# Kernel optimization log

Measured on AMD Instinct MI355X. Metric: run time of the kernel, lower is better.

## Reference

```python
import jax, jax.numpy as jnp
import numpy as np

Q = 8192      # num query tokens
S = 32768     # num support points
E = 131072    # num edges (query<-support neighbor pairs)
D = 256       # token_dim
H = 8         # num_heads
HD = D // H   # head_dim = 32
GEO = 128     # geo mlp_hidden = geo_dim
FFN = 2 * D   # ffn hidden
STAT_IN = 12  # 4 stats * 3 coords
EPS_LN = 1e-5


def gelu(x):
    return jax.nn.gelu(x, approximate=False)  # torch nn.GELU default (erf)


def layernorm(x, g, b):
    m = jnp.mean(x, axis=-1, keepdims=True)
    v = jnp.mean((x - m) ** 2, axis=-1, keepdims=True)
    return (x - m) * jax.lax.rsqrt(v + EPS_LN) * g + b


def setup_inputs() -> dict:
    key = jax.random.key(0)
    ks = jax.random.split(key, 16)
    w = lambda k, shp: jax.random.normal(k, shp, jnp.float32) * 0.02
    return {
        "query_tokens": jax.random.normal(ks[0], (Q, D), jnp.float32),
        "query_pos": jax.random.normal(ks[1], (Q, 3), jnp.float32),
        "support_feats": jax.random.normal(ks[2], (S, D), jnp.float32),
        "support_pos": jax.random.normal(ks[3], (S, 3), jnp.float32),
        "Wq": w(ks[4], (D, D)), "Wk": w(ks[5], (D, D)), "Wv": w(ks[6], (D, D)),
        "Wg": w(ks[7], (GEO, D)),
        "Wo": w(ks[8], (D, D)), "bo": jnp.zeros((D,), jnp.float32),
        "log_tau": jnp.array(0.0, jnp.float32),
        "ln1_g": jnp.ones((D,), jnp.float32), "ln1_b": jnp.zeros((D,), jnp.float32),
        "ln2_g": jnp.ones((D,), jnp.float32), "ln2_b": jnp.zeros((D,), jnp.float32),
        "Wf1": w(ks[9], (D, FFN)), "bf1": jnp.zeros((FFN,), jnp.float32),
        "Wf2": w(ks[10], (FFN, D)), "bf2": jnp.zeros((D,), jnp.float32),
        "Gw1": w(ks[11], (STAT_IN, GEO)), "Gb1": jnp.zeros((GEO,), jnp.float32),
        "Gw2": w(ks[12], (GEO, GEO)), "Gb2": jnp.zeros((GEO,), jnp.float32),
        "q_idx": jnp.sort(jax.random.randint(ks[13], (E,), 0, Q)),
        "s_idx": jax.random.randint(ks[14], (E,), 0, S),
        "num_queries": Q,
    }


def geo_stats(rel, q_idx, num_q):
    # rel: [E,3] relative positions; segmented mean/std/min/max -> [num_q, 12]
    ones = jnp.ones((rel.shape[0], 1), rel.dtype)
    cnt = jnp.maximum(jax.ops.segment_sum(ones, q_idx, num_q), 1.0)  # [Q,1]
    mean = jax.ops.segment_sum(rel, q_idx, num_q) / cnt
    var = jax.ops.segment_sum((rel - mean[q_idx]) ** 2, q_idx, num_q) / cnt
    std = jnp.sqrt(var)
    # torch inits min/max with +/-inf then clamps to [-100,100]; jax segment
    # min/max init with dtype extremes -> same result after clip
    mn = jnp.clip(jax.ops.segment_min(rel, q_idx, num_q), -100.0, 100.0)
    mx = jnp.clip(jax.ops.segment_max(rel, q_idx, num_q), -100.0, 100.0)
    return jnp.concatenate([mean, std, mn, mx], axis=-1)


def reference(query_tokens, query_pos, support_feats, support_pos,
              Wq, Wk, Wv, Wg, Wo, bo, log_tau,
              ln1_g, ln1_b, ln2_g, ln2_b,
              Wf1, bf1, Wf2, bf2, Gw1, Gb1, Gw2, Gb2,
              q_idx, s_idx, num_queries):
    num_q = num_queries
    # ---- statistical geo embedding ----
    rel = support_pos[s_idx] - query_pos[q_idx]                 # [E,3]
    raw = geo_stats(rel, q_idx, num_q)                          # [Q,12]
    geo = gelu(gelu(raw @ Gw1 + Gb1) @ Gw2 + Gb2)               # [Q,GEO]

    # ---- AGNO cross attention (pre-norm) ----
    qt = layernorm(query_tokens, ln1_g, ln1_b)
    Qf = qt @ Wq                                                # [Q,D]
    Kf = support_feats @ Wk                                     # [S,D]
    Vf = support_feats @ Wv                                     # [S,D]
    Gf = geo @ Wg                                               # [Q,D]
    qh = Qf[q_idx].reshape(E, H, HD)
    kh = Kf[s_idx].reshape(E, H, HD)
    vh = Vf[s_idx].reshape(E, H, HD)
    gh = Gf[q_idx].reshape(E, H, HD)
    tau = jnp.exp(log_tau)
    scores = jnp.sum(qh * kh, axis=-1) / (jnp.sqrt(jnp.float32(HD)) * tau)  # [E,H]
    # torch scores_max starts at 0 -> max(0, segment max)
    smax = jnp.maximum(jax.ops.segment_max(scores, q_idx, num_q), 0.0)
    ex = jnp.exp(scores - smax[q_idx])
    ssum = jax.ops.segment_sum(ex, q_idx, num_q)
    alpha = ex / jnp.maximum(ssum[q_idx], 1e-8)                 # [E,H]
    weighted = alpha[..., None] * (vh + gh)                     # [E,H,HD]
    out = jax.ops.segment_sum(weighted, q_idx, num_q)           # [Q,H,HD]
    attn = out.reshape(num_q, D) @ Wo + bo

    # ---- residual + FFN ----
    x = query_tokens + attn
    x = x + gelu(layernorm(x, ln2_g, ln2_b) @ Wf1 + bf1) @ Wf2 + bf2
    return x
```

## Files before the change

kernel.cpp:

```cpp
#include <hip/hip_runtime.h>
#include <math.h>

#define QN 8192
#define SN 32768
#define EN 131072
#define DN 256
#define HN 8
#define HDN 32
#define GEON 128
#define FFNN 512

typedef __attribute__((ext_vector_type(8))) short bf16x8;
typedef __attribute__((ext_vector_type(8))) unsigned short u16x8;
typedef __attribute__((ext_vector_type(4))) float f32x4;

__device__ __forceinline__ unsigned short f2b(float f) {
  union { float f; unsigned u; } v; v.f = f;
  unsigned u = v.u;
  u += 0x7fffu + ((u >> 16) & 1u);
  return (unsigned short)(u >> 16);
}
__device__ __forceinline__ float b2f(unsigned short h) {
  union { unsigned u; float f; } v; v.u = ((unsigned)h) << 16; return v.f;
}
// ... 34 lines not shown
    int k0 = (tile % ktiles) * 64, n0 = (tile / ktiles) * 64;
    int c4 = (t & 15) * 4;
    int r = t >> 4;
#pragma unroll
    for (int p = 0; p < 4; ++p) {
      int row = p * 16 + r;
      float4 v = *(const float4*)(src + (size_t)(k0 + row) * N + n0 + c4);
      ts[row][c4 + 0] = v.x; ts[row][c4 + 1] = v.y;
      ts[row][c4 + 2] = v.z; ts[row][c4 + 3] = v.w;
    }
    __syncthreads();
#pragma unroll
    for (int p = 0; p < 4; ++p) {
      int n = p * 16 + r;
      ushort4 o;
      o.x = f2b(ts[c4 + 0][n]); o.y = f2b(ts[c4 + 1][n]);
      o.z = f2b(ts[c4 + 2][n]); o.w = f2b(ts[c4 + 3][n]);
      *(ushort4*)(dst + (size_t)(n0 + n) * K + k0 + c4) = o;
    }
  } else if (b < 169) {
    int i = (b - 136) * 256 + t;
    if (i > QN) return;
    int lo = 0, hi = EN;
    while (lo < hi) {
      int mid = (lo + hi) >> 1;
      if (q_idx[mid] < i) lo = mid + 1; else hi = mid;
    }
    offs[i] = lo;
  } else {
    int row = (b - 169) * 4 + (t >> 6);
    int lane = t & 63;
    const float* xr = x_ln + (size_t)row * DN;
    float4 v = *(const float4*)(xr + lane * 4);
    float s = v.x + v.y + v.z + v.w;
    float ss = v.x * v.x + v.y * v.y + v.z * v.z + v.w * v.w;
#pragma unroll
    for (int msk = 1; msk <= 32; msk <<= 1) {
      s += __shfl_xor(s, msk);
      ss += __shfl_xor(ss, msk);
    }
    float mean = s * (1.f / 256.f);
    float var = ss * (1.f / 256.f) - mean * mean;
    float rs = 1.0f / sqrtf(var + 1e-5f);
    float4 gg = *(const float4*)(lng + lane * 4);
    float4 bb = *(const float4*)(lnb + lane * 4);
    unsigned short* o = ln_out + (size_t)row * DN + lane * 4;
    o[0] = f2b((v.x - mean) * rs * gg.x + bb.x);
    o[1] = f2b((v.y - mean) * rs * gg.y + bb.y);
    o[2] = f2b((v.z - mean) * rs * gg.z + bb.z);
    o[3] = f2b((v.w - mean) * rs * gg.w + bb.w);
  }
}

__global__ __launch_bounds__(256) void ln_kernel(
    const float* x, const float* g, const float* b, unsigned short* out) {
  int row = blockIdx.x * 4 + (threadIdx.x >> 6);
  int lane = threadIdx.x & 63;
  const float* xr = x + (size_t)row * DN;
  float4 v = *(const float4*)(xr + lane * 4);
  float s = v.x + v.y + v.z + v.w;
  float ss = v.x * v.x + v.y * v.y + v.z * v.z + v.w * v.w;
#pragma unroll
  for (int msk = 1; msk <= 32; msk <<= 1) {
    s += __shfl_xor(s, msk);
    ss += __shfl_xor(ss, msk);
  }
  float mean = s * (1.f / 256.f);
  float var = ss * (1.f / 256.f) - mean * mean;
  float rs = 1.0f / sqrtf(var + 1e-5f);
  float4 gg = *(const float4*)(g + lane * 4);
  float4 bb = *(const float4*)(b + lane * 4);
  unsigned short* o = out + (size_t)row * DN + lane * 4;
  o[0] = f2b((v.x - mean) * rs * gg.x + bb.x);
  o[1] = f2b((v.y - mean) * rs * gg.y + bb.y);
  o[2] = f2b((v.z - mean) * rs * gg.z + bb.z);
  o[3] = f2b((v.w - mean) * rs * gg.w + bb.w);
}


__device__ __forceinline__ void kv_body(
    char* smem, const float* A, const unsigned short* BT, unsigned short* KVb,
    int bm, int t) {
  unsigned short* As = (unsigned short*)smem;
  unsigned short* Bs = (unsigned short*)(smem + 32768);
  int w = t >> 6, lane = t & 63;
  int quad = lane >> 4, l16 = lane & 15;
  int wr = w >> 1, wc = w & 1;
  int srow = t >> 2, sub = t & 3;
  {
    const float* Ag = A + (size_t)(bm + srow) * 256 + sub * 64;
#pragma unroll
    for (int i = 0; i < 8; ++i) {
      float4 f0 = *(const float4*)(Ag + i * 8);
      float4 f1 = *(const float4*)(Ag + i * 8 + 4);
      u16x8 u;
      u[0] = f2b(f0.x); u[1] = f2b(f0.y); u[2] = f2b(f0.z); u[3] = f2b(f0.w);
      u[4] = f2b(f1.x); u[5] = f2b(f1.y); u[6] = f2b(f1.z); u[7] = f2b(f1.w);
      *lds_gk<256>(As, srow, sub * 64 + i * 8) = u;
    }
  }
  int brow = t >> 3, bsub = t & 7;
  u16x8 pre[4];
  {
    const unsigned short* Bg = BT + (size_t)brow * 256 + bsub * 32;
#pragma unroll
    for (int i = 0; i < 4; ++i) pre[i] = *reinterpret_cast<const u16x8*>(Bg + i * 8);
  }
  for (int ct = 0; ct < 16; ++ct) {
#pragma unroll
    for (int i = 0; i < 4; ++i)
      *lds_gk<256>(Bs, brow, bsub * 32 + i * 8) = pre[i];
    __syncthreads();
    if (ct < 15) {
      const unsigned short* Bg = BT + (size_t)((ct + 1) * 32 + brow) * 256 + bsub * 32;
#pragma unroll
      for (int i = 0; i < 4; ++i) pre[i] = *reinterpret_cast<const u16x8*>(Bg + i * 8);
    }
    f32x4 acc[2];
    acc[0] = (f32x4){0.f, 0.f, 0.f, 0.f};
    acc[1] = (f32x4){0.f, 0.f, 0.f, 0.f};
#pragma unroll
    for (int k = 0; k < 8; ++k) {
      bf16x8 a0 = *reinterpret_cast<bf16x8*>(lds_gk<256>(As, wr * 32 + l16, k * 32 + quad * 8));
      bf16x8 a1 = *reinterpret_cast<bf16x8*>(lds_gk<256>(As, wr * 32 + 16 + l16, k * 32 + quad * 8));
      bf16x8 b0 = *reinterpret_cast<bf16x8*>(lds_gk<256>(Bs, wc * 16 + l16, k * 32 + quad * 8));
      acc[0] = __builtin_amdgcn_mfma_f32_16x16x32_bf16(a0, b0, acc[0], 0, 0, 0);
      acc[1] = __builtin_amdgcn_mfma_f32_16x16x32_bf16(a1, b0, acc[1], 0, 0, 0);
    }
#pragma unroll
    for (int i = 0; i < 2; ++i)
#pragma unroll
      for (int r = 0; r < 4; ++r) {
        int rw = bm + wr * 32 + i * 16 + quad * 4 + r;
        int col = ct * 32 + wc * 16 + l16;
        KVb[(size_t)rw * 512 + col] = f2b(acc[i][r]);
      }
    __syncthreads();
  }
}

template <bool A_FP32, bool HAS_BIAS, bool DO_GELU, bool HAS_RESID, bool STORE_F32>
__device__ __forceinline__ void gemm64_body(
    char* smem, const void* Ap, const unsigned short* BT, int N, int K,
    const float* bias, const float* resid, float* outF, unsigned short* outB,
    int bm, int bn, int t) {
  unsigned short (*As)[40] = (unsigned short(*)[40])smem;
  unsigned short (*Bs)[40] = (unsigned short(*)[40])(smem + 5120);
  int w = t >> 6, lane = t & 63;
  int wr = w >> 1, wc = w & 1;
  int quad = lane >> 4, l16 = lane & 15;
  int row = t >> 2, chunk = t & 3;

  const float* AgF = (const float*)Ap + (size_t)(bm + row) * K + chunk * 8;
  const unsigned short* AgB = (const unsigned short*)Ap + (size_t)(bm + row) * K + chunk * 8;
  const unsigned short* Bg = BT + (size_t)(bn + row) * K + chunk * 8;

  float4 pf0, pf1;
  u16x8 pa, pb;
  if (A_FP32) { pf0 = *(const float4*)AgF; pf1 = *(const float4*)(AgF + 4); }
  else        { pa = *(const u16x8*)AgB; }
  pb = *(const u16x8*)Bg;

  f32x4 acc[2][2];
#pragma unroll
  for (int i = 0; i < 2; ++i)
#pragma unroll
    for (int j = 0; j < 2; ++j) acc[i][j] = (f32x4){0.f, 0.f, 0.f, 0.f};

  for (int k0 = 0; k0 < K; k0 += 32) {
    u16x8 ua;
    if (A_FP32) {
      ua[0] = f2b(pf0.x); ua[1] = f2b(pf0.y); ua[2] = f2b(pf0.z); ua[3] = f2b(pf0.w);
      ua[4] = f2b(pf1.x); ua[5] = f2b(pf1.y); ua[6] = f2b(pf1.z); ua[7] = f2b(pf1.w);
    } else {
      ua = pa;
    }
    *reinterpret_cast<u16x8*>(&As[row][chunk * 8]) = ua;
    *reinterpret_cast<u16x8*>(&Bs[row][chunk * 8]) = pb;
    __syncthreads();
    if (k0 + 32 < K) {
      if (A_FP32) { pf0 = *(const float4*)(AgF + k0 + 32); pf1 = *(const float4*)(AgF + k0 + 36); }
      else        { pa = *(const u16x8*)(AgB + k0 + 32); }
      pb = *(const u16x8*)(Bg + k0 + 32);
    }
    bf16x8 a0 = *reinterpret_cast<const bf16x8*>(&As[wr * 32 + l16][quad * 8]);
    bf16x8 a1 = *reinterpret_cast<const bf16x8*>(&As[wr * 32 + 16 + l16][quad * 8]);
    bf16x8 b0 = *reinterpret_cast<const bf16x8*>(&Bs[wc * 32 + l16][quad * 8]);
    bf16x8 b1 = *reinterpret_cast<const bf16x8*>(&Bs[wc * 32 + 16 + l16][quad * 8]);
    acc[0][0] = __builtin_amdgcn_mfma_f32_16x16x32_bf16(a0, b0, acc[0][0], 0, 0, 0);
    acc[0][1] = __builtin_amdgcn_mfma_f32_16x16x32_bf16(a0, b1, acc[0][1], 0, 0, 0);
    acc[1][0] = __builtin_amdgcn_mfma_f32_16x16x32_bf16(a1, b0, acc[1][0], 0, 0, 0);
    acc[1][1] = __builtin_amdgcn_mfma_f32_16x16x32_bf16(a1, b1, acc[1][1], 0, 0, 0);
    __syncthreads();
  }

#pragma unroll
  for (int i = 0; i < 2; ++i)
#pragma unroll
    for (int j = 0; j < 2; ++j) {
      int col = bn + wc * 32 + j * 16 + l16;
      float bv = HAS_BIAS ? bias[col] : 0.f;
#pragma unroll
      for (int r = 0; r < 4; ++r) {
        int rw = bm + wr * 32 + i * 16 + quad * 4 + r;
        float v = acc[i][j][r] + bv;
        if (DO_GELU) v = gelu_f(v);
        if (HAS_RESID) v += resid[(size_t)rw * N + col];
        if (STORE_F32) outF[(size_t)rw * N + col] = v;
        else outB[(size_t)rw * N + col] = f2b(v);
      }
    }
}

__device__ __forceinline__ void geo_body(
    char* smem, const float* qpos, const float* spos, const int* offs,
    const int* s_idx, const float* Gw1, const float* Gb1,
    const float* Gw2, const float* Gb2, const unsigned short* WgT,
    unsigned short* Gf_b, int qb, int t) {
  float (*rs)[12] = (float(*)[12])smem;
  unsigned short* geoL = (unsigned short*)(smem + 3072);
  float (*h1)[128] = (float(*)[128])(smem + 19456);
  unsigned short* Bs = (unsigned short*)(smem + 19456);

  {
    int q = qb + (t >> 2);
    int sub = t & 3;
    int e0 = offs[q], e1 = offs[q + 1];
    float qx = qpos[q * 3 + 0], qy = qpos[q * 3 + 1], qz = qpos[q * 3 + 2];
    float cnt = 0.f, sx = 0.f, sy = 0.f, sz = 0.f, sxx = 0.f, syy = 0.f, szz = 0.f;
    float mnx = 1e30f, mny = 1e30f, mnz = 1e30f, mxx = -1e30f, mxy = -1e30f, mxz = -1e30f;
    for (int e = e0 + sub; e < e1; e += 4) {
      int s = s_idx[e];
      float rx = spos[s * 3 + 0] - qx;
      float ry = spos[s * 3 + 1] - qy;
      float rz = spos[s * 3 + 2] - qz;
      cnt += 1.f;
      sx += rx; sy += ry; sz += rz;
      sxx += rx * rx; syy += ry * ry; szz += rz * rz;
      mnx = fminf(mnx, rx); mny = fminf(mny, ry); mnz = fminf(mnz, rz);
      mxx = fmaxf(mxx, rx); mxy = fmaxf(mxy, ry); mxz = fmaxf(mxz, rz);
    }
#pragma unroll
    for (int msk = 1; msk <= 2; msk <<= 1) {
      cnt += __shfl_xor(cnt, msk);
      sx += __shfl_xor(sx, msk); sy += __shfl_xor(sy, msk); sz += __shfl_xor(sz, msk);
      sxx += __shfl_xor(sxx, msk); syy += __shfl_xor(syy, msk); szz += __shfl_xor(szz, msk);
      mnx = fminf(mnx, __shfl_xor(mnx, msk));
      mny = fminf(mny, __shfl_xor(mny, msk));
      mnz = fminf(mnz, __shfl_xor(mnz, msk));
      mxx = fmaxf(mxx, __shfl_xor(mxx, msk));
      mxy = fmaxf(mxy, __shfl_xor(mxy, msk));
      mxz = fmaxf(mxz, __shfl_xor(mxz, msk));
    }
    if (sub == 0) {
      int qq = t >> 2;
      float c = fmaxf(cnt, 1.f);
      float mx_ = sx / c, my_ = sy / c, mz_ = sz / c;
      float vx = fmaxf(sxx / c - mx_ * mx_, 0.f);
      float vy = fmaxf(syy / c - my_ * my_, 0.f);
      float vz = fmaxf(szz / c - mz_ * mz_, 0.f);
      rs[qq][0] = mx_; rs[qq][1] = my_; rs[qq][2] = mz_;
      rs[qq][3] = sqrtf(vx); rs[qq][4] = sqrtf(vy); rs[qq][5] = sqrtf(vz);
      rs[qq][6] = fminf(fmaxf(mnx, -100.f), 100.f);
      rs[qq][7] = fminf(fmaxf(mny, -100.f), 100.f);
      rs[qq][8] = fminf(fmaxf(mnz, -100.f), 100.f);
      rs[qq][9] = fminf(fmaxf(mxx, -100.f), 100.f);
      rs[qq][10] = fminf(fmaxf(mxy, -100.f), 100.f);
      rs[qq][11] = fminf(fmaxf(mxz, -100.f), 100.f);
    }
  }
  __syncthreads();

  {
    int j = t & 127;
    int grp = t >> 7;
    int qbase = grp * 32;
    float acc[32];
    float b1 = Gb1[j];
#pragma unroll
    for (int qq = 0; qq < 32; ++qq) acc[qq] = b1;
    for (int i = 0; i < 12; ++i) {
      float wv = Gw1[i * GEON + j];
#pragma unroll
      for (int qq = 0; qq < 32; ++qq) acc[qq] += rs[qbase + qq][i] * wv;
    }
#pragma unroll
    for (int qq = 0; qq < 32; ++qq) h1[qbase + qq][j] = gelu_f(acc[qq]);
    __syncthreads();
    float b2 = Gb2[j];
    float acc2[32];
#pragma unroll
    for (int qq = 0; qq < 32; ++qq) acc2[qq] = b2;
    for (int k = 0; k < 128; ++k) {
      float wv = Gw2[k * GEON + j];
#pragma unroll
      for (int qq = 0; qq < 32; ++qq) acc2[qq] += h1[qbase + qq][k] * wv;
    }
#pragma unroll
    for (int qq = 0; qq < 32; ++qq)
      *lds_gs128(geoL, qbase + qq, j) = f2b(gelu_f(acc2[qq]));
  }
  __syncthreads();

  {
    int w = t >> 6, lane = t & 63;
    int wr = w >> 1, wc = w & 1;
    int quad = lane >> 4, l16 = lane & 15;
    int row = t >> 2, sub = t & 3;
    for (int ct = 0; ct < 4; ++ct) {
      int bn = ct * 64;
      {
        const unsigned short* Bg = WgT + (size_t)(bn + row) * 128 + sub * 32;
#pragma unroll
        for (int i = 0; i < 4; ++i)
          *lds_gk<128>(Bs, row, sub * 32 + i * 8) = *reinterpret_cast<const u16x8*>(Bg + i * 8);
      }
      __syncthreads();
      f32x4 acc[2][2];
#pragma unroll
      for (int i = 0; i < 2; ++i)
#pragma unroll
        for (int j = 0; j < 2; ++j) acc[i][j] = (f32x4){0.f, 0.f, 0.f, 0.f};
#pragma unroll
      for (int k = 0; k < 4; ++k) {
        bf16x8 a0 = *reinterpret_cast<bf16x8*>(lds_gk<128>(geoL, wr * 32 + l16, k * 32 + quad * 8));
        bf16x8 a1 = *reinterpret_cast<bf16x8*>(lds_gk<128>(geoL, wr * 32 + 16 + l16, k * 32 + quad * 8));
        bf16x8 b0 = *reinterpret_cast<bf16x8*>(lds_gk<128>(Bs, wc * 32 + l16, k * 32 + quad * 8));
        bf16x8 b1 = *reinterpret_cast<bf16x8*>(lds_gk<128>(Bs, wc * 32 + 16 + l16, k * 32 + quad * 8));
        acc[0][0] = __builtin_amdgcn_mfma_f32_16x16x32_bf16(a0, b0, acc[0][0], 0, 0, 0);
        acc[0][1] = __builtin_amdgcn_mfma_f32_16x16x32_bf16(a0, b1, acc[0][1], 0, 0, 0);
        acc[1][0] = __builtin_amdgcn_mfma_f32_16x16x32_bf16(a1, b0, acc[1][0], 0, 0, 0);
        acc[1][1] = __builtin_amdgcn_mfma_f32_16x16x32_bf16(a1, b1, acc[1][1], 0, 0, 0);
      }
#pragma unroll
      for (int i = 0; i < 2; ++i)
#pragma unroll
        for (int j = 0; j < 2; ++j) {
          int col = bn + wc * 32 + j * 16 + l16;
#pragma unroll
          for (int r = 0; r < 4; ++r) {
            int rw = qb + wr * 32 + i * 16 + quad * 4 + r;
            Gf_b[(size_t)rw * 256 + col] = f2b(acc[i][j][r]);
          }
        }
      __syncthreads();
    }
  }
}

__global__ __launch_bounds__(256) void fused_stage2(
    const float* qpos, const float* spos, const int* offs, const int* s_idx,
    const float* Gw1, const float* Gb1, const float* Gw2, const float* Gb2,
    const unsigned short* WgT, unsigned short* Gf_b,
    const float* support_feats, const unsigned short* WkvT, unsigned short* KVb,
    const unsigned short* qt_b, const unsigned short* WqT, unsigned short* Qb) {
  __shared__ __align__(16) char smem[52224];
  int b = blockIdx.x;
  int t = threadIdx.x;
  if (b < 128) {
    geo_body(smem, qpos, spos, offs, s_idx, Gw1, Gb1, Gw2, Gb2, WgT, Gf_b, b * 64, t);
  } else if (b < 640) {
    kv_body(smem, support_feats, WkvT, KVb, (b - 128) * 64, t);
  } else {
    int bb = b - 640;
    int bm = (bb & 127) * 64, bn = (bb >> 7) * 64;
    gemm64_body<false, false, false, false, false>(
        smem, qt_b, WqT, DN, 256, nullptr, nullptr, nullptr, Qb, bm, bn, t);
  }
}

template <bool A_FP32, bool HAS_BIAS, bool DO_GELU, bool HAS_RESID, bool STORE_F32>
__global__ __launch_bounds__(256) void gemm64(
    const void* Ap, const unsigned short* BT, int N, int K,
    const float* bias, const float* resid, float* outF, unsigned short* outB) {
  __shared__ __align__(16) char smem[10240];
  gemm64_body<A_FP32, HAS_BIAS, DO_GELU, HAS_RESID, STORE_F32>(
      smem, Ap, BT, N, K, bias, resid, outF, outB,
      blockIdx.x * 64, blockIdx.y * 64, threadIdx.x);
}

__global__ __launch_bounds__(256) void attn_edge_kernel(
    const unsigned short* Qb, const unsigned short* Gfb, const unsigned short* KVb,
    const int* s_idx, const int* offs, const float* log_tau, unsigned short* attn_b) {
  int q = blockIdx.x * 4 + (threadIdx.x >> 6);
  int lane = threadIdx.x & 63;
  int slot = lane >> 4;
  int sl = lane & 15;
  int d0 = sl * 16;
  int e0 = offs[q], e1 = offs[q + 1];
  float invs = expf(-log_tau[0]) * 0.17677669529663687f;
  u16x8 qu0 = *(const u16x8*)(Qb + (size_t)q * DN + d0);
  u16x8 qu1 = *(const u16x8*)(Qb + (size_t)q * DN + d0 + 8);
  u16x8 gu0 = *(const u16x8*)(Gfb + (size_t)q * DN + d0);
  u16x8 gu1 = *(const u16x8*)(Gfb + (size_t)q * DN + d0 + 8);
  float qf[16], gf[16];
#pragma unroll
  for (int j = 0; j < 8; ++j) {
    qf[j] = b2f(qu0[j]) * invs; qf[j + 8] = b2f(qu1[j]) * invs;
    gf[j] = b2f(gu0[j]);        gf[j + 8] = b2f(gu1[j]);
  }
  const float NEG = -1e30f;
  float m = -INFINITY, l = 0.f;
  float a[16];
#pragma unroll
  for (int j = 0; j < 16; ++j) a[j] = 0.f;
  for (int e = e0; e < e1; e += 4) {
    int ee = e + slot;
    bool valid = ee < e1;
    int s = s_idx[valid ? ee : (e1 - 1)];
    const unsigned short* kr = KVb + (size_t)s * 512 + d0;
    u16x8 ku0 = *(const u16x8*)kr;
    u16x8 ku1 = *(const u16x8*)(kr + 8);
    u16x8 vu0 = *(const u16x8*)(kr + 256);
    u16x8 vu1 = *(const u16x8*)(kr + 264);
    float p = 0.f;
#pragma unroll
    for (int j = 0; j < 8; ++j) {
      p += qf[j] * b2f(ku0[j]);
      p += qf[j + 8] * b2f(ku1[j]);
    }
    p += __shfl_xor(p, 1);
    if (!valid) p = -INFINITY;
    float mnew = fmaxf(m, p);
    float sc = (m > NEG) ? __expf(m - mnew) : 0.f;
    float we = valid ? __expf(p - mnew) : 0.f;
    l = l * sc + we;
#pragma unroll
    for (int j = 0; j < 8; ++j) {
      a[j] = a[j] * sc + we * b2f(vu0[j]);
      a[j + 8] = a[j + 8] * sc + we * b2f(vu1[j]);
    }
    m = mnew;
  }
#pragma unroll
  for (int msk = 16; msk <= 32; msk <<= 1) {
    float om = __shfl_xor(m, msk);
    float ol = __shfl_xor(l, msk);
    float M2 = fmaxf(m, om);
    float ws = (m > NEG) ? __expf(m - M2) : 0.f;
    float wo = (om > NEG) ? __expf(om - M2) : 0.f;
    l = l * ws + ol * wo;
#pragma unroll
    for (int j = 0; j < 16; ++j) {
      float oa = __shfl_xor(a[j], msk);
      a[j] = a[j] * ws + oa * wo;
    }
    m = M2;
  }
  float M = fmaxf(m, 0.f);
  float em = (m > NEG) ? __expf(m - M) : 0.f;
  float denom = fmaxf(l * em, 1e-8f);
  float f = em / denom;
  float sa = l * f;
  if (slot == 0) {
    u16x8 o0, o1;
#pragma unroll
    for (int j = 0; j < 8; ++j) {
      o0[j] = f2b(a[j] * f + gf[j] * sa);
      o1[j] = f2b(a[j + 8] * f + gf[j + 8] * sa);
    }
    *(u16x8*)(attn_b + (size_t)q * DN + d0) = o0;
    *(u16x8*)(attn_b + (size_t)q * DN + d0 + 8) = o1;
  }
}

extern "C" void kernel_launch(void* const* d_in, const int* in_sizes, int n_in,
                              void* d_out, int out_size, void* d_ws, size_t ws_size,
                              hipStream_t stream) {
  const float* query_tokens  = (const float*)d_in[0];
  const float* query_pos     = (const float*)d_in[1];
  const float* support_feats = (const float*)d_in[2];
  const float* support_pos   = (const float*)d_in[3];
  const float* Wq  = (const float*)d_in[4];
  const float* Wk  = (const float*)d_in[5];
  const float* Wv  = (const float*)d_in[6];
  const float* Wg  = (const float*)d_in[7];
  const float* Wo  = (const float*)d_in[8];
  const float* bo  = (const float*)d_in[9];
  const float* log_tau = (const float*)d_in[10];
  const float* ln1_g = (const float*)d_in[11];
  const float* ln1_b = (const float*)d_in[12];
  const float* ln2_g = (const float*)d_in[13];
  const float* ln2_b = (const float*)d_in[14];
  const float* Wf1 = (const float*)d_in[15];
  const float* bf1 = (const float*)d_in[16];
  const float* Wf2 = (const float*)d_in[17];
  const float* bf2 = (const float*)d_in[18];
  const float* Gw1 = (const float*)d_in[19];
  const float* Gb1 = (const float*)d_in[20];
  const float* Gw2 = (const float*)d_in[21];
  const float* Gb2 = (const float*)d_in[22];
  const int* q_idx = (const int*)d_in[23];
  const int* s_idx = (const int*)d_in[24];
  float* out = (float*)d_out;

  char* ws = (char*)d_ws;
  size_t off = 0;
  auto alloc = [&](size_t bytes) -> void* {
    void* p = ws + off;
    off = (off + bytes + 255) & ~(size_t)255;
    return p;
  };
  unsigned short* WqT  = (unsigned short*)alloc(65536 * 2);
  unsigned short* WkvT = (unsigned short*)alloc(131072 * 2);
  unsigned short* WgT  = (unsigned short*)alloc(32768 * 2);
  unsigned short* WoT  = (unsigned short*)alloc(65536 * 2);
  unsigned short* Wf1T = (unsigned short*)alloc(131072 * 2);
  unsigned short* Wf2T = (unsigned short*)alloc(131072 * 2);
  int* offs            = (int*)alloc((QN + 1) * 4);
  unsigned short* qt_b  = (unsigned short*)alloc((size_t)QN * DN * 2);
  unsigned short* Qb    = (unsigned short*)alloc((size_t)QN * DN * 2);
  unsigned short* Gf_b  = (unsigned short*)alloc((size_t)QN * DN * 2);
  unsigned short* KVb   = (unsigned short*)alloc((size_t)SN * 512 * 2);
  unsigned short* attn_b = (unsigned short*)alloc((size_t)QN * DN * 2);
  float* x1             = (float*)alloc((size_t)QN * DN * 4);
  unsigned short* z_b   = (unsigned short*)alloc((size_t)QN * DN * 2);
  unsigned short* h_b   = (unsigned short*)alloc((size_t)QN * FFNN * 2);

  fused_prep<<<2217, 256, 0, stream>>>(Wq, Wk, Wv, Wg, Wo, Wf1, Wf2,
                                       WqT, WkvT, WgT, WoT, Wf1T, Wf2T,
                                       q_idx, offs,
                                       query_tokens, ln1_g, ln1_b, qt_b);
  fused_stage2<<<1152, 256, 0, stream>>>(query_pos, support_pos, offs, s_idx,
                                         Gw1, Gb1, Gw2, Gb2, WgT, Gf_b,
                                         support_feats, WkvT, KVb,
                                         qt_b, WqT, Qb);
  attn_edge_kernel<<<QN / 4, 256, 0, stream>>>(Qb, Gf_b, KVb, s_idx, offs, log_tau, attn_b);
  gemm64<false, true, false, true, true><<<dim3(QN / 64, DN / 64), 256, 0, stream>>>(
      attn_b, WoT, DN, 256, bo, query_tokens, x1, nullptr);
  ln_kernel<<<QN / 4, 256, 0, stream>>>(x1, ln2_g, ln2_b, z_b);
  gemm64<false, true, true, false, false><<<dim3(QN / 64, FFNN / 64), 256, 0, stream>>>(
      z_b, Wf1T, FFNN, 256, bf1, nullptr, nullptr, h_b);
  gemm64<false, true, false, true, true><<<dim3(QN / 64, DN / 64), 256, 0, stream>>>(
      h_b, Wf2T, DN, 512, bf2, x1, out, nullptr);

  (void)in_sizes; (void)n_in; (void)out_size; (void)ws_size;
}
```

Measured before the change: 240.1 us.

## Shrink KV tiles, deepen GEMM K-step, and split geo MLP to cut LDS

The KV projection tile shrinks from 64 to 32 rows per block, which doubles the number of KV blocks. It also swaps the MFMA operands so each lane writes four contiguous bf16 outputs in one vector store. The generic 64x64 GEMM now stages 64 K-elements per sync instead of 32, which halves the number of barriers but increases its LDS use. The geo MLP processes its 64 queries in two halves of 16 per thread group, reducing register and LDS footprint so the fused stage2 shared buffer can shrink from about 52KB to 35KB and more blocks can reside per CU.

```diff
diff --git a/kernel.cpp b/kernel.cpp
--- a/kernel.cpp
+++ b/kernel.cpp
@@ -140,59 +140,58 @@
     char* smem, const float* A, const unsigned short* BT, unsigned short* KVb,
     int bm, int t) {
   unsigned short* As = (unsigned short*)smem;
-  unsigned short* Bs = (unsigned short*)(smem + 32768);
+  unsigned short* Bs = (unsigned short*)(smem + 16384);
   int w = t >> 6, lane = t & 63;
   int quad = lane >> 4, l16 = lane & 15;
   int wr = w >> 1, wc = w & 1;
-  int srow = t >> 2, sub = t & 3;
+  int arow = t >> 3, asub = t & 7;
   {
-    const float* Ag = A + (size_t)(bm + srow) * 256 + sub * 64;
-#pragma unroll
-    for (int i = 0; i < 8; ++i) {
-      float4 f0 = *(const float4*)(Ag + i * 8);
-      float4 f1 = *(const float4*)(Ag + i * 8 + 4);
-      u16x8 u;
-      u[0] = f2b(f0.x); u[1] = f2b(f0.y); u[2] = f2b(f0.z); u[3] = f2b(f0.w);
-      u[4] = f2b(f1.x); u[5] = f2b(f1.y); u[6] = f2b(f1.z); u[7] = f2b(f1.w);
-      *lds_gk<256>(As, srow, sub * 64 + i * 8) = u;
-    }
-  }
-  int brow = t >> 3, bsub = t & 7;
+    const float* Ag = A + (size_t)(bm + arow) * 256 + asub * 32;
+#pragma unroll
+    for (int i = 0; i < 2; ++i) {
+      float4 f0 = *(const float4*)(Ag + i * 16);
+      float4 f1 = *(const float4*)(Ag + i * 16 + 4);
+      float4 f2 = *(const float4*)(Ag + i * 16 + 8);
+      float4 f3 = *(const float4*)(Ag + i * 16 + 12);
+      u16x8 u0, u1;
+      u0[0] = f2b(f0.x); u0[1] = f2b(f0.y); u0[2] = f2b(f0.z); u0[3] = f2b(f0.w);
+      u0[4] = f2b(f1.x); u0[5] = f2b(f1.y); u0[6] = f2b(f1.z); u0[7] = f2b(f1.w);
+      u1[0] = f2b(f2.x); u1[1] = f2b(f2.y); u1[2] = f2b(f2.z); u1[3] = f2b(f2.w);
+      u1[4] = f2b(f3.x); u1[5] = f2b(f3.y); u1[6] = f2b(f3.z); u1[7] = f2b(f3.w);
+      *lds_gk<256>(As, arow, asub * 32 + i * 16) = u0;
+      *lds_gk<256>(As, arow, asub * 32 + i * 16 + 8) = u1;
+    }
+  }
   u16x8 pre[4];
   {
-    const unsigned short* Bg = BT + (size_t)brow * 256 + bsub * 32;
+    const unsigned short* Bg = BT + (size_t)arow * 256 + asub * 32;
 #pragma unroll
     for (int i = 0; i < 4; ++i) pre[i] = *reinterpret_cast<const u16x8*>(Bg + i * 8);
   }
   for (int ct = 0; ct < 16; ++ct) {
 #pragma unroll
     for (int i = 0; i < 4; ++i)
-      *lds_gk<256>(Bs, brow, bsub * 32 + i * 8) = pre[i];
+      *lds_gk<256>(Bs, arow, asub * 32 + i * 8) = pre[i];
     __syncthreads();
     if (ct < 15) {
-      const unsigned short* Bg = BT + (size_t)((ct + 1) * 32 + brow) * 256 + bsub * 32;
+      const unsigned short* Bg = BT + (size_t)((ct + 1) * 32 + arow) * 256 + asub * 32;
 #pragma unroll
       for (int i = 0; i < 4; ++i) pre[i] = *reinterpret_cast<const u16x8*>(Bg + i * 8);
     }
-    f32x4 acc[2];
-    acc[0] = (f32x4){0.f, 0.f, 0.f, 0.f};
-    acc[1] = (f32x4){0.f, 0.f, 0.f, 0.f};
+    f32x4 acc = (f32x4){0.f, 0.f, 0.f, 0.f};
 #pragma unroll
     for (int k = 0; k < 8; ++k) {
-      bf16x8 a0 = *reinterpret_cast<bf16x8*>(lds_gk<256>(As, wr * 32 + l16, k * 32 + quad * 8));
-      bf16x8 a1 = *reinterpret_cast<bf16x8*>(lds_gk<256>(As, wr * 32 + 16 + l16, k * 32 + quad * 8));
-      bf16x8 b0 = *reinterpret_cast<bf16x8*>(lds_gk<256>(Bs, wc * 16 + l16, k * 32 + quad * 8));
-      acc[0] = __builtin_amdgcn_mfma_f32_16x16x32_bf16(a0, b0, acc[0], 0, 0, 0);
-      acc[1] = __builtin_amdgcn_mfma_f32_16x16x32_bf16(a1, b0, acc[1], 0, 0, 0);
-    }
-#pragma unroll
-    for (int i = 0; i < 2; ++i)
-#pragma unroll
-      for (int r = 0; r < 4; ++r) {
-        int rw = bm + wr * 32 + i * 16 + quad * 4 + r;
-        int col = ct * 32 + wc * 16 + l16;
-        KVb[(size_t)rw * 512 + col] = f2b(acc[i][r]);
-      }
+      bf16x8 a = *reinterpret_cast<bf16x8*>(lds_gk<256>(As, wr * 16 + l16, k * 32 + quad * 8));
+      bf16x8 b = *reinterpret_cast<bf16x8*>(lds_gk<256>(Bs, wc * 16 + l16, k * 32 + quad * 8));
+      acc = __builtin_amdgcn_mfma_f32_16x16x32_bf16(b, a, acc, 0, 0, 0);
+    }
+    {
+      int rw = bm + wr * 16 + l16;
+      int c0 = ct * 32 + wc * 16 + quad * 4;
+      ushort4 o;
+      o.x = f2b(acc[0]); o.y = f2b(acc[1]); o.z = f2b(acc[2]); o.w = f2b(acc[3]);
+      *(ushort4*)(KVb + (size_t)rw * 512 + c0) = o;
+    }
     __syncthreads();
   }
 }
@@ -202,22 +201,26 @@
     char* smem, const void* Ap, const unsigned short* BT, int N, int K,
     const float* bias, const float* resid, float* outF, unsigned short* outB,
     int bm, int bn, int t) {
-  unsigned short (*As)[40] = (unsigned short(*)[40])smem;
-  unsigned short (*Bs)[40] = (unsigned short(*)[40])(smem + 5120);
+  unsigned short* As = (unsigned short*)smem;
+  unsigned short* Bs = (unsigned short*)(smem + 9216);
   int w = t >> 6, lane = t & 63;
   int wr = w >> 1, wc = w & 1;
   int quad = lane >> 4, l16 = lane & 15;
-  int row = t >> 2, chunk = t & 3;
-
-  const float* AgF = (const float*)Ap + (size_t)(bm + row) * K + chunk * 8;
-  const unsigned short* AgB = (const unsigned short*)Ap + (size_t)(bm + row) * K + chunk * 8;
-  const unsigned short* Bg = BT + (size_t)(bn + row) * K + chunk * 8;
-
-  float4 pf0, pf1;
-  u16x8 pa, pb;
-  if (A_FP32) { pf0 = *(const float4*)AgF; pf1 = *(const float4*)(AgF + 4); }
-  else        { pa = *(const u16x8*)AgB; }
-  pb = *(const u16x8*)Bg;
+  int row = t >> 2, sub = t & 3;
+
+  const float* AgF = (const float*)Ap + (size_t)(bm + row) * K + sub * 16;
+  const unsigned short* AgB = (const unsigned short*)Ap + (size_t)(bm + row) * K + sub * 16;
+  const unsigned short* Bg = BT + (size_t)(bn + row) * K + sub * 16;
+
+  float4 pf[4];
+  u16x8 pa[2], pb[2];
+  if (A_FP32) {
+    pf[0] = *(const float4*)AgF;        pf[1] = *(const float4*)(AgF + 4);
+    pf[2] = *(const float4*)(AgF + 8);  pf[3] = *(const float4*)(AgF + 12);
+  } else {
+    pa[0] = *(const u16x8*)AgB; pa[1] = *(const u16x8*)(AgB + 8);
+  }
+  pb[0] = *(const u16x8*)Bg; pb[1] = *(const u16x8*)(Bg + 8);
 
   f32x4 acc[2][2];
 #pragma unroll
@@ -225,30 +228,42 @@
 #pragma unroll
     for (int j = 0; j < 2; ++j) acc[i][j] = (f32x4){0.f, 0.f, 0.f, 0.f};
 
-  for (int k0 = 0; k0 < K; k0 += 32) {
-    u16x8 ua;
+  for (int k0 = 0; k0 < K; k0 += 64) {
     if (A_FP32) {
-      ua[0] = f2b(pf0.x); ua[1] = f2b(pf0.y); ua[2] = f2b(pf0.z); ua[3] = f2b(pf0.w);
-      ua[4] = f2b(pf1.x); ua[5] = f2b(pf1.y); ua[6] = f2b(pf1.z); ua[7] = f2b(pf1.w);
+      u16x8 u0, u1;
+      u0[0] = f2b(pf[0].x); u0[1] = f2b(pf[0].y); u0[2] = f2b(pf[0].z); u0[3] = f2b(pf[0].w);
+      u0[4] = f2b(pf[1].x); u0[5] = f2b(pf[1].y); u0[6] = f2b(pf[1].z); u0[7] = f2b(pf[1].w);
+      u1[0] = f2b(pf[2].x); u1[1] = f2b(pf[2].y); u1[2] = f2b(pf[2].z); u1[3] = f2b(pf[2].w);
+      u1[4] = f2b(pf[3].x); u1[5] = f2b(pf[3].y); u1[6] = f2b(pf[3].z); u1[7] = f2b(pf[3].w);
+      *reinterpret_cast<u16x8*>(&As[row * 72 + sub * 16]) = u0;
+      *reinterpret_cast<u16x8*>(&As[row * 72 + sub * 16 + 8]) = u1;
     } else {
-      ua = pa;
-    }
-    *reinterpret_cast<u16x8*>(&As[row][chunk * 8]) = ua;
-    *reinterpret_cast<u16x8*>(&Bs[row][chunk * 8]) = pb;
+      *reinterpret_cast<u16x8*>(&As[row * 72 + sub * 16]) = pa[0];
+      *reinterpret_cast<u16x8*>(&As[row * 72 + sub * 16 + 8]) = pa[1];
+    }
+    *reinterpret_cast<u16x8*>(&Bs[row * 72 + sub * 16]) = pb[0];
+    *reinterpret_cast<u16x8*>(&Bs[row * 72 + sub * 16 + 8]) = pb[1];
     __syncthreads();
-    if (k0 + 32 < K) {
-      if (A_FP32) { pf0 = *(const float4*)(AgF + k0 + 32); pf1 = *(const float4*)(AgF + k0 + 36); }
-      else        { pa = *(const u16x8*)(AgB + k0 + 32); }
-      pb = *(const u16x8*)(Bg + k0 + 32);
-    }
-    bf16x8 a0 = *reinterpret_cast<const bf16x8*>(&As[wr * 32 + l16][quad * 8]);
-    bf16x8 a1 = *reinterpret_cast<const bf16x8*>(&As[wr * 32 + 16 + l16][quad * 8]);
-    bf16x8 b0 = *reinterpret_cast<const bf16x8*>(&Bs[wc * 32 + l16][quad * 8]);
-    bf16x8 b1 = *reinterpret_cast<const bf16x8*>(&Bs[wc * 32 + 16 + l16][quad * 8]);
-    acc[0][0] = __builtin_amdgcn_mfma_f32_16x16x32_bf16(a0, b0, acc[0][0], 0, 0, 0);
-    acc[0][1] = __builtin_amdgcn_mfma_f32_16x16x32_bf16(a0, b1, acc[0][1], 0, 0, 0);
-    acc[1][0] = __builtin_amdgcn_mfma_f32_16x16x32_bf16(a1, b0, acc[1][0], 0, 0, 0);
-    acc[1][1] = __builtin_amdgcn_mfma_f32_16x16x32_bf16(a1, b1, acc[1][1], 0, 0, 0);
+    if (k0 + 64 < K) {
+      if (A_FP32) {
+        pf[0] = *(const float4*)(AgF + k0 + 64);  pf[1] = *(const float4*)(AgF + k0 + 68);
+        pf[2] = *(const float4*)(AgF + k0 + 72);  pf[3] = *(const float4*)(AgF + k0 + 76);
+      } else {
+        pa[0] = *(const u16x8*)(AgB + k0 + 64); pa[1] = *(const u16x8*)(AgB + k0 + 72);
+      }
+      pb[0] = *(const u16x8*)(Bg + k0 + 64); pb[1] = *(const u16x8*)(Bg + k0 + 72);
+    }
+#pragma unroll
+    for (int ks = 0; ks < 2; ++ks) {
+      bf16x8 a0 = *reinterpret_cast<const bf16x8*>(&As[(wr * 32 + l16) * 72 + ks * 32 + quad * 8]);
+      bf16x8 a1 = *reinterpret_cast<const bf16x8*>(&As[(wr * 32 + 16 + l16) * 72 + ks * 32 + quad * 8]);
+      bf16x8 b0 = *reinterpret_cast<const bf16x8*>(&Bs[(wc * 32 + l16) * 72 + ks * 32 + quad * 8]);
+      bf16x8 b1 = *reinterpret_cast<const bf16x8*>(&Bs[(wc * 32 + 16 + l16) * 72 + ks * 32 + quad * 8]);
+      acc[0][0] = __builtin_amdgcn_mfma_f32_16x16x32_bf16(a0, b0, acc[0][0], 0, 0, 0);
+      acc[0][1] = __builtin_amdgcn_mfma_f32_16x16x32_bf16(a0, b1, acc[0][1], 0, 0, 0);
+      acc[1][0] = __builtin_amdgcn_mfma_f32_16x16x32_bf16(a1, b0, acc[1][0], 0, 0, 0);
+      acc[1][1] = __builtin_amdgcn_mfma_f32_16x16x32_bf16(a1, b1, acc[1][1], 0, 0, 0);
+    }
     __syncthreads();
   }
 
@@ -277,7 +292,7 @@
     unsigned short* Gf_b, int qb, int t) {
   float (*rs)[12] = (float(*)[12])smem;
   unsigned short* geoL = (unsigned short*)(smem + 3072);
-  float (*h1)[128] = (float(*)[128])(smem + 19456);
+  float* h1 = (float*)(smem + 19456);
   unsigned short* Bs = (unsigned short*)(smem + 19456);
 
   {
@@ -332,33 +347,36 @@
   {
     int j = t & 127;
     int grp = t >> 7;
-    int qbase = grp * 32;
-    float acc[32];
-    float b1 = Gb1[j];
-#pragma unroll
-    for (int qq = 0; qq < 32; ++qq) acc[qq] = b1;
-    for (int i = 0; i < 12; ++i) {
-      float wv = Gw1[i * GEON + j];
-#pragma unroll
-      for (int qq = 0; qq < 32; ++qq) acc[qq] += rs[qbase + qq][i] * wv;
-    }
-#pragma unroll
-    for (int qq = 0; qq < 32; ++qq) h1[qbase + qq][j] = gelu_f(acc[qq]);
-    __syncthreads();
-    float b2 = Gb2[j];
-    float acc2[32];
-#pragma unroll
-    for (int qq = 0; qq < 32; ++qq) acc2[qq] = b2;
-    for (int k = 0; k < 128; ++k) {
-      float wv = Gw2[k * GEON + j];
-#pragma unroll
-      for (int qq = 0; qq < 32; ++qq) acc2[qq] += h1[qbase + qq][k] * wv;
-    }
-#pragma unroll
-    for (int qq = 0; qq < 32; ++qq)
-      *lds_gs128(geoL, qbase + qq, j) = f2b(gelu_f(acc2[qq]));
-  }
-  __syncthreads();
+    for (int half = 0; half < 2; ++half) {
+      int qloc = grp * 16;
+      int qglob = half * 32 + qloc;
+      float acc[16];
+      float b1 = Gb1[j];
+#pragma unroll
+      for (int qq = 0; qq < 16; ++qq) acc[qq] = b1;
+      for (int i = 0; i < 12; ++i) {
+        float wv = Gw1[i * GEON + j];
+#pragma unroll
+        for (int qq = 0; qq < 16; ++qq) acc[qq] += rs[qglob + qq][i] * wv;
+      }
+#pragma unroll
+      for (int qq = 0; qq < 16; ++qq) h1[(qloc + qq) * 128 + j] = gelu_f(acc[qq]);
+      __syncthreads();
+      float acc2[16];
+      float b2 = Gb2[j];
+#pragma unroll
+      for (int qq = 0; qq < 16; ++qq) acc2[qq] = b2;
+      for (int k = 0; k < 128; ++k) {
+        float wv = Gw2[k * GEON + j];
+#pragma unroll
+        for (int qq = 0; qq < 16; ++qq) acc2[qq] += h1[(qloc + qq) * 128 + k] * wv;
+      }
+#pragma unroll
+      for (int qq = 0; qq < 16; ++qq)
+        *lds_gs128(geoL, qglob + qq, j) = f2b(gelu_f(acc2[qq]));
+      __syncthreads();
+    }
+  }
 
   {
     int w = t >> 6, lane = t & 63;
@@ -412,15 +430,15 @@
     const unsigned short* WgT, unsigned short* Gf_b,
     const float* support_feats, const unsigned short* WkvT, unsigned short* KVb,
     const unsigned short* qt_b, const unsigned short* WqT, unsigned short* Qb) {
-  __shared__ __align__(16) char smem[52224];
+  __shared__ __align__(16) char smem[35840];
   int b = blockIdx.x;
   int t = threadIdx.x;
   if (b < 128) {
     geo_body(smem, qpos, spos, offs, s_idx, Gw1, Gb1, Gw2, Gb2, WgT, Gf_b, b * 64, t);
-  } else if (b < 640) {
-    kv_body(smem, support_feats, WkvT, KVb, (b - 128) * 64, t);
+  } else if (b < 1152) {
+    kv_body(smem, support_feats, WkvT, KVb, (b - 128) * 32, t);
   } else {
-    int bb = b - 640;
+    int bb = b - 1152;
     int bm = (bb & 127) * 64, bn = (bb >> 7) * 64;
     gemm64_body<false, false, false, false, false>(
         smem, qt_b, WqT, DN, 256, nullptr, nullptr, nullptr, Qb, bm, bn, t);
@@ -431,7 +449,7 @@
 __global__ __launch_bounds__(256) void gemm64(
     const void* Ap, const unsigned short* BT, int N, int K,
     const float* bias, const float* resid, float* outF, unsigned short* outB) {
-  __shared__ __align__(16) char smem[10240];
+  __shared__ __align__(16) char smem[18432];
   gemm64_body<A_FP32, HAS_BIAS, DO_GELU, HAS_RESID, STORE_F32>(
       smem, Ap, BT, N, K, bias, resid, outF, outB,
       blockIdx.x * 64, blockIdx.y * 64, threadIdx.x);
@@ -579,7 +597,7 @@
                                        WqT, WkvT, WgT, WoT, Wf1T, Wf2T,
                                        q_idx, offs,
                                        query_tokens, ln1_g, ln1_b, qt_b);
-  fused_stage2<<<1152, 256, 0, stream>>>(query_pos, support_pos, offs, s_idx,
+  fused_stage2<<<1664, 256, 0, stream>>>(query_pos, support_pos, offs, s_idx,
                                          Gw1, Gb1, Gw2, Gb2, WgT, Gf_b,
                                          support_feats, WkvT, KVb,
                                          qt_b, WqT, Qb);
```

After: 249.7 us. 4.0% more time.

## Read weight tiles directly from global memory and stage full-K A tiles in LDS

Applied to the files above, without the earlier changes.

The GEMM bodies (KV projection, geo Wg projection and the generic 64x64 GEMM) no longer stage the transposed weight (B) tiles through LDS. Each wave loads its B fragments straight from global/L2, and the whole K-extent of the A tile is loaded into LDS once, so the per-k-step syncthreads are removed. The geo MLP is split into two halves to shrink the h1 buffer, which lowers the fused_stage2 LDS footprint and may allow higher occupancy. The cost is uncoalesced-ish global fragment loads for B that depend on L2 hits, and a larger LDS footprint for the K=512 GEMM.

```diff
diff --git a/kernel.cpp b/kernel.cpp
--- a/kernel.cpp
+++ b/kernel.cpp
@@ -140,7 +140,6 @@
     char* smem, const float* A, const unsigned short* BT, unsigned short* KVb,
     int bm, int t) {
   unsigned short* As = (unsigned short*)smem;
-  unsigned short* Bs = (unsigned short*)(smem + 32768);
   int w = t >> 6, lane = t & 63;
   int quad = lane >> 4, l16 = lane & 15;
   int wr = w >> 1, wc = w & 1;
@@ -157,101 +156,68 @@
       *lds_gk<256>(As, srow, sub * 64 + i * 8) = u;
     }
   }
-  int brow = t >> 3, bsub = t & 7;
-  u16x8 pre[4];
-  {
-    const unsigned short* Bg = BT + (size_t)brow * 256 + bsub * 32;
-#pragma unroll
-    for (int i = 0; i < 4; ++i) pre[i] = *reinterpret_cast<const u16x8*>(Bg + i * 8);
+  __syncthreads();
+  bf16x8 af0[8], af1[8];
+#pragma unroll
+  for (int k = 0; k < 8; ++k) {
+    af0[k] = *reinterpret_cast<bf16x8*>(lds_gk<256>(As, wr * 32 + l16, k * 32 + quad * 8));
+    af1[k] = *reinterpret_cast<bf16x8*>(lds_gk<256>(As, wr * 32 + 16 + l16, k * 32 + quad * 8));
   }
   for (int ct = 0; ct < 16; ++ct) {
-#pragma unroll
-    for (int i = 0; i < 4; ++i)
-      *lds_gk<256>(Bs, brow, bsub * 32 + i * 8) = pre[i];
-    __syncthreads();
-    if (ct < 15) {
-      const unsigned short* Bg = BT + (size_t)((ct + 1) * 32 + brow) * 256 + bsub * 32;
-#pragma unroll
-      for (int i = 0; i < 4; ++i) pre[i] = *reinterpret_cast<const u16x8*>(Bg + i * 8);
-    }
-    f32x4 acc[2];
-    acc[0] = (f32x4){0.f, 0.f, 0.f, 0.f};
-    acc[1] = (f32x4){0.f, 0.f, 0.f, 0.f};
+    const unsigned short* Brow = BT + (size_t)(ct * 32 + wc * 16 + l16) * 256 + quad * 8;
+    f32x4 acc0 = (f32x4){0.f, 0.f, 0.f, 0.f};
+    f32x4 acc1 = (f32x4){0.f, 0.f, 0.f, 0.f};
 #pragma unroll
     for (int k = 0; k < 8; ++k) {
-      bf16x8 a0 = *reinterpret_cast<bf16x8*>(lds_gk<256>(As, wr * 32 + l16, k * 32 + quad * 8));
-      bf16x8 a1 = *reinterpret_cast<bf16x8*>(lds_gk<256>(As, wr * 32 + 16 + l16, k * 32 + quad * 8));
-      bf16x8 b0 = *reinterpret_cast<bf16x8*>(lds_gk<256>(Bs, wc * 16 + l16, k * 32 + quad * 8));
-      acc[0] = __builtin_amdgcn_mfma_f32_16x16x32_bf16(a0, b0, acc[0], 0, 0, 0);
-      acc[1] = __builtin_amdgcn_mfma_f32_16x16x32_bf16(a1, b0, acc[1], 0, 0, 0);
-    }
-#pragma unroll
-    for (int i = 0; i < 2; ++i)
-#pragma unroll
-      for (int r = 0; r < 4; ++r) {
-        int rw = bm + wr * 32 + i * 16 + quad * 4 + r;
-        int col = ct * 32 + wc * 16 + l16;
-        KVb[(size_t)rw * 512 + col] = f2b(acc[i][r]);
-      }
-    __syncthreads();
-  }
-}
-
-template <bool A_FP32, bool HAS_BIAS, bool DO_GELU, bool HAS_RESID, bool STORE_F32>
+      bf16x8 b = *reinterpret_cast<const bf16x8*>(Brow + k * 32);
+      acc0 = __builtin_amdgcn_mfma_f32_16x16x32_bf16(af0[k], b, acc0, 0, 0, 0);
+      acc1 = __builtin_amdgcn_mfma_f32_16x16x32_bf16(af1[k], b, acc1, 0, 0, 0);
+    }
+    int col = ct * 32 + wc * 16 + l16;
+#pragma unroll
+    for (int r = 0; r < 4; ++r) {
+      KVb[(size_t)(bm + wr * 32 + quad * 4 + r) * 512 + col] = f2b(acc0[r]);
+      KVb[(size_t)(bm + wr * 32 + 16 + quad * 4 + r) * 512 + col] = f2b(acc1[r]);
+    }
+  }
+}
+
+template <int KT, bool HAS_BIAS, bool DO_GELU, bool HAS_RESID, bool STORE_F32>
 __device__ __forceinline__ void gemm64_body(
-    char* smem, const void* Ap, const unsigned short* BT, int N, int K,
+    char* smem, const unsigned short* A, const unsigned short* BT, int N,
     const float* bias, const float* resid, float* outF, unsigned short* outB,
     int bm, int bn, int t) {
-  unsigned short (*As)[40] = (unsigned short(*)[40])smem;
-  unsigned short (*Bs)[40] = (unsigned short(*)[40])(smem + 5120);
+  unsigned short* As = (unsigned short*)smem;
   int w = t >> 6, lane = t & 63;
   int wr = w >> 1, wc = w & 1;
   int quad = lane >> 4, l16 = lane & 15;
-  int row = t >> 2, chunk = t & 3;
-
-  const float* AgF = (const float*)Ap + (size_t)(bm + row) * K + chunk * 8;
-  const unsigned short* AgB = (const unsigned short*)Ap + (size_t)(bm + row) * K + chunk * 8;
-  const unsigned short* Bg = BT + (size_t)(bn + row) * K + chunk * 8;
-
-  float4 pf0, pf1;
-  u16x8 pa, pb;
-  if (A_FP32) { pf0 = *(const float4*)AgF; pf1 = *(const float4*)(AgF + 4); }
-  else        { pa = *(const u16x8*)AgB; }
-  pb = *(const u16x8*)Bg;
-
+  int row = t >> 2, sub = t & 3;
+  constexpr int CH = KT / 4;
+  {
+    const unsigned short* Ag = A + (size_t)(bm + row) * KT + sub * CH;
+#pragma unroll
+    for (int i = 0; i < CH / 8; ++i)
+      *lds_gk<KT>(As, row, sub * CH + i * 8) = *reinterpret_cast<const u16x8*>(Ag + i * 8);
+  }
+  __syncthreads();
+  const unsigned short* Bg0 = BT + (size_t)(bn + wc * 32 + l16) * KT + quad * 8;
+  const unsigned short* Bg1 = BT + (size_t)(bn + wc * 32 + 16 + l16) * KT + quad * 8;
   f32x4 acc[2][2];
 #pragma unroll
   for (int i = 0; i < 2; ++i)
 #pragma unroll
     for (int j = 0; j < 2; ++j) acc[i][j] = (f32x4){0.f, 0.f, 0.f, 0.f};
-
-  for (int k0 = 0; k0 < K; k0 += 32) {
-    u16x8 ua;
-    if (A_FP32) {
-      ua[0] = f2b(pf0.x); ua[1] = f2b(pf0.y); ua[2] = f2b(pf0.z); ua[3] = f2b(pf0.w);
-      ua[4] = f2b(pf1.x); ua[5] = f2b(pf1.y); ua[6] = f2b(pf1.z); ua[7] = f2b(pf1.w);
-    } else {
-      ua = pa;
-    }
-    *reinterpret_cast<u16x8*>(&As[row][chunk * 8]) = ua;
-    *reinterpret_cast<u16x8*>(&Bs[row][chunk * 8]) = pb;
-    __syncthreads();
-    if (k0 + 32 < K) {
-      if (A_FP32) { pf0 = *(const float4*)(AgF + k0 + 32); pf1 = *(const float4*)(AgF + k0 + 36); }
-      else        { pa = *(const u16x8*)(AgB + k0 + 32); }
-      pb = *(const u16x8*)(Bg + k0 + 32);
-    }
-    bf16x8 a0 = *reinterpret_cast<const bf16x8*>(&As[wr * 32 + l16][quad * 8]);
-    bf16x8 a1 = *reinterpret_cast<const bf16x8*>(&As[wr * 32 + 16 + l16][quad * 8]);
-    bf16x8 b0 = *reinterpret_cast<const bf16x8*>(&Bs[wc * 32 + l16][quad * 8]);
-    bf16x8 b1 = *reinterpret_cast<const bf16x8*>(&Bs[wc * 32 + 16 + l16][quad * 8]);
+#pragma unroll
+  for (int k0 = 0; k0 < KT; k0 += 32) {
+    bf16x8 a0 = *reinterpret_cast<bf16x8*>(lds_gk<KT>(As, wr * 32 + l16, k0 + quad * 8));
+    bf16x8 a1 = *reinterpret_cast<bf16x8*>(lds_gk<KT>(As, wr * 32 + 16 + l16, k0 + quad * 8));
+    bf16x8 b0 = *reinterpret_cast<const bf16x8*>(Bg0 + k0);
+    bf16x8 b1 = *reinterpret_cast<const bf16x8*>(Bg1 + k0);
     acc[0][0] = __builtin_amdgcn_mfma_f32_16x16x32_bf16(a0, b0, acc[0][0], 0, 0, 0);
     acc[0][1] = __builtin_amdgcn_mfma_f32_16x16x32_bf16(a0, b1, acc[0][1], 0, 0, 0);
     acc[1][0] = __builtin_amdgcn_mfma_f32_16x16x32_bf16(a1, b0, acc[1][0], 0, 0, 0);
     acc[1][1] = __builtin_amdgcn_mfma_f32_16x16x32_bf16(a1, b1, acc[1][1], 0, 0, 0);
-    __syncthreads();
-  }
-
+  }
 #pragma unroll
   for (int i = 0; i < 2; ++i)
 #pragma unroll
@@ -277,8 +243,7 @@
     unsigned short* Gf_b, int qb, int t) {
   float (*rs)[12] = (float(*)[12])smem;
   unsigned short* geoL = (unsigned short*)(smem + 3072);
-  float (*h1)[128] = (float(*)[128])(smem + 19456);
-  unsigned short* Bs = (unsigned short*)(smem + 19456);
+  float* h1 = (float*)(smem + 19456);
 
   {
     int q = qb + (t >> 2);
@@ -332,48 +297,45 @@
   {
     int j = t & 127;
     int grp = t >> 7;
-    int qbase = grp * 32;
-    float acc[32];
-    float b1 = Gb1[j];
-#pragma unroll
-    for (int qq = 0; qq < 32; ++qq) acc[qq] = b1;
-    for (int i = 0; i < 12; ++i) {
-      float wv = Gw1[i * GEON + j];
-#pragma unroll
-      for (int qq = 0; qq < 32; ++qq) acc[qq] += rs[qbase + qq][i] * wv;
-    }
-#pragma unroll
-    for (int qq = 0; qq < 32; ++qq) h1[qbase + qq][j] = gelu_f(acc[qq]);
-    __syncthreads();
-    float b2 = Gb2[j];
-    float acc2[32];
-#pragma unroll
-    for (int qq = 0; qq < 32; ++qq) acc2[qq] = b2;
-    for (int k = 0; k < 128; ++k) {
-      float wv = Gw2[k * GEON + j];
-#pragma unroll
-      for (int qq = 0; qq < 32; ++qq) acc2[qq] += h1[qbase + qq][k] * wv;
-    }
-#pragma unroll
-    for (int qq = 0; qq < 32; ++qq)
-      *lds_gs128(geoL, qbase + qq, j) = f2b(gelu_f(acc2[qq]));
-  }
-  __syncthreads();
+    for (int half = 0; half < 2; ++half) {
+      int qloc = grp * 16;
+      int qglob = half * 32 + qloc;
+      float acc[16];
+      float b1 = Gb1[j];
+#pragma unroll
+      for (int qq = 0; qq < 16; ++qq) acc[qq] = b1;
+      for (int i = 0; i < 12; ++i) {
+        float wv = Gw1[i * GEON + j];
+#pragma unroll
+        for (int qq = 0; qq < 16; ++qq) acc[qq] += rs[qglob + qq][i] * wv;
+      }
+#pragma unroll
+      for (int qq = 0; qq < 16; ++qq) h1[(qloc + qq) * 128 + j] = gelu_f(acc[qq]);
+      __syncthreads();
+      float acc2[16];
+      float b2 = Gb2[j];
+#pragma unroll
+      for (int qq = 0; qq < 16; ++qq) acc2[qq] = b2;
+      for (int k = 0; k < 128; ++k) {
+        float wv = Gw2[k * GEON + j];
+#pragma unroll
+        for (int qq = 0; qq < 16; ++qq) acc2[qq] += h1[(qloc + qq) * 128 + k] * wv;
+      }
+#pragma unroll
+      for (int qq = 0; qq < 16; ++qq)
+        *lds_gs128(geoL, qglob + qq, j) = f2b(gelu_f(acc2[qq]));
+      __syncthreads();
+    }
+  }
 
   {
     int w = t >> 6, lane = t & 63;
     int wr = w >> 1, wc = w & 1;
     int quad = lane >> 4, l16 = lane & 15;
-    int row = t >> 2, sub = t & 3;
     for (int ct = 0; ct < 4; ++ct) {
       int bn = ct * 64;
-      {
-        const unsigned short* Bg = WgT + (size_t)(bn + row) * 128 + sub * 32;
-#pragma unroll
-        for (int i = 0; i < 4; ++i)
-          *lds_gk<128>(Bs, row, sub * 32 + i * 8) = *reinterpret_cast<const u16x8*>(Bg + i * 8);
-      }
-      __syncthreads();
+      const unsigned short* Bg0 = WgT + (size_t)(bn + wc * 32 + l16) * 128 + quad * 8;
+      const unsigned short* Bg1 = WgT + (size_t)(bn + wc * 32 + 16 + l16) * 128 + quad * 8;
       f32x4 acc[2][2];
 #pragma unroll
       for (int i = 0; i < 2; ++i)
@@ -383,8 +345,8 @@
       for (int k = 0; k < 4; ++k) {
         bf16x8 a0 = *reinterpret_cast<bf16x8*>(lds_gk<128>(geoL, wr * 32 + l16, k * 32 + quad * 8));
         bf16x8 a1 = *reinterpret_cast<bf16x8*>(lds_gk<128>(geoL, wr * 32 + 16 + l16, k * 32 + quad * 8));
-        bf16x8 b0 = *reinterpret_cast<bf16x8*>(lds_gk<128>(Bs, wc * 32 + l16, k * 32 + quad * 8));
-        bf16x8 b1 = *reinterpret_cast<bf16x8*>(lds_gk<128>(Bs, wc * 32 + 16 + l16, k * 32 + quad * 8));
+        bf16x8 b0 = *reinterpret_cast<const bf16x8*>(Bg0 + k * 32);
+        bf16x8 b1 = *reinterpret_cast<const bf16x8*>(Bg1 + k * 32);
         acc[0][0] = __builtin_amdgcn_mfma_f32_16x16x32_bf16(a0, b0, acc[0][0], 0, 0, 0);
         acc[0][1] = __builtin_amdgcn_mfma_f32_16x16x32_bf16(a0, b1, acc[0][1], 0, 0, 0);
         acc[1][0] = __builtin_amdgcn_mfma_f32_16x16x32_bf16(a1, b0, acc[1][0], 0, 0, 0);
@@ -401,7 +363,6 @@
             Gf_b[(size_t)rw * 256 + col] = f2b(acc[i][j][r]);
           }
         }
-      __syncthreads();
     }
   }
 }
@@ -412,7 +373,7 @@
     const unsigned short* WgT, unsigned short* Gf_b,
     const float* support_feats, const unsigned short* WkvT, unsigned short* KVb,
     const unsigned short* qt_b, const unsigned short* WqT, unsigned short* Qb) {
-  __shared__ __align__(16) char smem[52224];
+  __shared__ __align__(16) char smem[35840];
   int b = blockIdx.x;
   int t = threadIdx.x;
   if (b < 128) {
@@ -422,18 +383,18 @@
   } else {
     int bb = b - 640;
     int bm = (bb & 127) * 64, bn = (bb >> 7) * 64;
-    gemm64_body<false, false, false, false, false>(
-        smem, qt_b, WqT, DN, 256, nullptr, nullptr, nullptr, Qb, bm, bn, t);
-  }
-}
-
-template <bool A_FP32, bool HAS_BIAS, bool DO_GELU, bool HAS_RESID, bool STORE_F32>
+    gemm64_body<256, false, false, false, false>(
+        smem, qt_b, WqT, DN, nullptr, nullptr, nullptr, Qb, bm, bn, t);
+  }
+}
+
+template <int KT, bool HAS_BIAS, bool DO_GELU, bool HAS_RESID, bool STORE_F32>
 __global__ __launch_bounds__(256) void gemm64(
-    const void* Ap, const unsigned short* BT, int N, int K,
+    const unsigned short* A, const unsigned short* BT, int N,
     const float* bias, const float* resid, float* outF, unsigned short* outB) {
-  __shared__ __align__(16) char smem[10240];
-  gemm64_body<A_FP32, HAS_BIAS, DO_GELU, HAS_RESID, STORE_F32>(
-      smem, Ap, BT, N, K, bias, resid, outF, outB,
+  __shared__ __align__(16) char smem[64 * KT * 2];
+  gemm64_body<KT, HAS_BIAS, DO_GELU, HAS_RESID, STORE_F32>(
+      smem, A, BT, N, bias, resid, outF, outB,
       blockIdx.x * 64, blockIdx.y * 64, threadIdx.x);
 }
 
@@ -584,13 +545,13 @@
                                          support_feats, WkvT, KVb,
                                          qt_b, WqT, Qb);
   attn_edge_kernel<<<QN / 4, 256, 0, stream>>>(Qb, Gf_b, KVb, s_idx, offs, log_tau, attn_b);
-  gemm64<false, true, false, true, true><<<dim3(QN / 64, DN / 64), 256, 0, stream>>>(
-      attn_b, WoT, DN, 256, bo, query_tokens, x1, nullptr);
+  gemm64<256, true, false, true, true><<<dim3(QN / 64, DN / 64), 256, 0, stream>>>(
+      attn_b, WoT, DN, bo, query_tokens, x1, nullptr);
   ln_kernel<<<QN / 4, 256, 0, stream>>>(x1, ln2_g, ln2_b, z_b);
-  gemm64<false, true, true, false, false><<<dim3(QN / 64, FFNN / 64), 256, 0, stream>>>(
-      z_b, Wf1T, FFNN, 256, bf1, nullptr, nullptr, h_b);
-  gemm64<false, true, false, true, true><<<dim3(QN / 64, DN / 64), 256, 0, stream>>>(
-      h_b, Wf2T, DN, 512, bf2, x1, out, nullptr);
+  gemm64<256, true, true, false, false><<<dim3(QN / 64, FFNN / 64), 256, 0, stream>>>(
+      z_b, Wf1T, FFNN, bf1, nullptr, nullptr, h_b);
+  gemm64<512, true, false, true, true><<<dim3(QN / 64, DN / 64), 256, 0, stream>>>(
+      h_b, Wf2T, DN, bf2, x1, out, nullptr);
 
   (void)in_sizes; (void)n_in; (void)out_size; (void)ws_size;
 }
```

Result: slower. 265.7 us (+10.7%).
